# Kernel optimization log

Hardware: AMD Instinct MI355X
Metric: run time of the kernel (lower is better)

## Reference

```python
import jax, jax.numpy as jnp
import numpy as np


def _gelu(x):
    # torch.nn.functional.gelu default: exact erf form
    return jax.nn.gelu(x, approximate=False)


def setup_inputs() -> dict:
    key = jax.random.key(0)
    ks = jax.random.split(key, 6)
    B, L, H, MAXLEN = 8, 2048, 1024, 256
    former_input = jax.random.normal(ks[0], (B, L, H), dtype=jnp.float32)
    hidden_sates = jax.random.normal(ks[1], (B, L, H), dtype=jnp.float32)
    token_type_ids = jax.random.randint(ks[2], (B, L), 0, MAXLEN, dtype=jnp.int32)
    attention_mask = jnp.ones((B, L), dtype=jnp.float32)
    # learned params (init.normal_ std=0.02, biases zero)
    W_down = jax.random.normal(ks[3], (2 * H, H), dtype=jnp.float32) * 0.02
    b_down = jnp.zeros((H,), dtype=jnp.float32)
    W_row = jax.random.normal(ks[4], (H, H), dtype=jnp.float32) * 0.02
    b_row = jnp.zeros((H,), dtype=jnp.float32)
    return {
        "former_input": former_input,
        "hidden_sates": hidden_sates,
        "token_type_ids": token_type_ids,
        "attention_mask": attention_mask,
        "W_down": W_down,
        "b_down": b_down,
        "W_row": W_row,
        "b_row": b_row,
        "max_length": 256,
    }


def reference(former_input, hidden_sates, token_type_ids, attention_mask,
              W_down, b_down, W_row, b_row, max_length):
    # down_proj + gelu: [B, L, 2H] @ [2H, H] -> [B, L, H]
    x = jnp.concatenate([former_input, hidden_sates], axis=-1)
    sequence_output = _gelu(jnp.einsum("blf,fh->blh", x, W_down) + b_down)

    # one_hot_from @ sequence_output == segment-sum of tokens into table cells
    # cell_hidden[b, t] = sum_{l : token_type_ids[b,l]==t} sequence_output[b, l]
    seg = jax.vmap(lambda vals, ids: jax.ops.segment_sum(vals, ids, num_segments=max_length))
    cell_hidden = seg(sequence_output, token_type_ids)  # [B, max_length, H]

    # row_linear + gelu (dropout is identity in eval mode)
    cell_hidden = _gelu(jnp.einsum("bth,hk->btk", cell_hidden, W_row) + b_row)

    # one_hot_to @ cell_hidden == gather cell back to each token position
    seq_hidden = jnp.take_along_axis(
        cell_hidden, token_type_ids[:, :, None].astype(jnp.int32), axis=1
    )  # [B, L, H]
    return seq_hidden
```

## Files before the change

kernel.cpp:

```cpp
#include <hip/hip_runtime.h>

typedef unsigned short ushort_t;
typedef __bf16 bf16x8 __attribute__((ext_vector_type(8)));
typedef float f32x4 __attribute__((ext_vector_type(4)));

__device__ __forceinline__ unsigned short f2bf(float f) {
    unsigned u = __float_as_uint(f);
    u += 0x7fffu + ((u >> 16) & 1u);
    return (unsigned short)(u >> 16);
}
__device__ __forceinline__ float bf2f(unsigned short h) {
    return __uint_as_float(((unsigned)h) << 16);
}
__device__ __forceinline__ float gelu_f(float x) {
    return 0.5f * x * (1.0f + erff(x * 0.70710678118654752440f));
}

__global__ void prep_kernel(const float4* __restrict__ former,
                            const float4* __restrict__ hidden,
                            uint4* __restrict__ Xb4,
                            const float* __restrict__ Wd, ushort_t* __restrict__ WdT,
                            const float* __restrict__ Wr, ushort_t* __restrict__ WrT)
{
    const int blk = blockIdx.x;
    const int tid = threadIdx.x;
    if (blk < 16384) {
        const int row = blk;
        const float4* src = (tid < 128)
            ? (former + (size_t)row * 256 + (tid & 127) * 2)
            : (hidden + (size_t)row * 256 + (tid & 127) * 2);
        float4 a = src[0], b = src[1];
        uint4 o;
        o.x = f2bf(a.x) | ((unsigned)f2bf(a.y) << 16);
        o.y = f2bf(a.z) | ((unsigned)f2bf(a.w) << 16);
        o.z = f2bf(b.x) | ((unsigned)f2bf(b.y) << 16);
        o.w = f2bf(b.z) | ((unsigned)f2bf(b.w) << 16);
        Xb4[(size_t)row * 256 + tid] = o;
    } else {
        __shared__ float tile[32][33];
        const float* W; ushort_t* Wt; int R, C, b;
        if (blk < 16384 + 2048) { b = blk - 16384; W = Wd; Wt = WdT; R = 2048; C = 1024; }
        else                    { b = blk - 18432; W = Wr; Wt = WrT; R = 1024; C = 1024; }
        const int bx = (b & 31) * 32;
        const int by = (b >> 5) * 32;
        const int tx = tid & 31, ty = tid >> 5;
        #pragma unroll
        for (int j = 0; j < 32; j += 8)
            tile[ty + j][tx] = W[(size_t)(by + ty + j) * C + bx + tx];
        __syncthreads();
        #pragma unroll
        for (int j = 0; j < 32; j += 8)
            Wt[(size_t)(bx + ty + j) * R + by + tx] = f2bf(tile[tx][ty + j]);
    }
}

template <bool OUT_BF16>
__global__ void gemm_bias_gelu_kernel(const ushort_t* __restrict__ A,
                                      const ushort_t* __restrict__ Bt,
                                      const float* __restrict__ bias,
                                      void* __restrict__ C,
                                      int M, int N, int K)
{
    __shared__ __align__(16) ushort_t sA[128 * 64];
    __shared__ __align__(16) ushort_t sB[128 * 64];
    const int tid  = threadIdx.x;
    const int lane = tid & 63;
    const int wave = tid >> 6;
    const int wm = (wave & 1) * 64;
    const int wn = (wave >> 1) * 64;
    const long bm = (long)blockIdx.x * 128;
    const long bn = (long)blockIdx.y * 128;

    f32x4 acc[4][4] = {};

    const int srow = wave * 8 + (lane >> 3);
    const int scol = ((lane & 7) ^ (lane >> 3)) * 8;
    const int ldsbase = wave * 512;

    for (int k0 = 0; k0 < K; k0 += 64) {
        __syncthreads();
        #pragma unroll
        for (int it = 0; it < 4; ++it) {
            const ushort_t* gA = A + (size_t)(bm + it * 32 + srow) * K + k0 + scol;
            const ushort_t* gB = Bt + (size_t)(bn + it * 32 + srow) * K + k0 + scol;
            __builtin_amdgcn_global_load_lds(
                (__attribute__((address_space(1))) void*)gA,
                (__attribute__((address_space(3))) void*)&sA[ldsbase + it * 2048], 16, 0, 0);
            __builtin_amdgcn_global_load_lds(
                (__attribute__((address_space(1))) void*)gB,
                (__attribute__((address_space(3))) void*)&sB[ldsbase + it * 2048], 16, 0, 0);
        }
        __syncthreads();

        const int arow = wm + (lane & 15);
        const int brow = wn + (lane & 15);
        const int sw = lane & 7;
        const int cbase = lane >> 4;
        #pragma unroll
        for (int kk = 0; kk < 64; kk += 32) {
            const int koff = (((kk >> 3) + cbase) ^ sw) << 3;
            bf16x8 af[4], bfr[4];
            #pragma unroll
            for (int t = 0; t < 4; ++t) {
                af[t]  = *(const bf16x8*)&sA[(arow + t * 16) * 64 + koff];
                bfr[t] = *(const bf16x8*)&sB[(brow + t * 16) * 64 + koff];
            }
            #pragma unroll
            for (int i = 0; i < 4; ++i)
                #pragma unroll
                for (int j = 0; j < 4; ++j)
                    acc[i][j] = __builtin_amdgcn_mfma_f32_16x16x32_bf16(af[i], bfr[j], acc[i][j], 0, 0, 0);
        }
    }

    #pragma unroll
    for (int i = 0; i < 4; ++i) {
        const long row0 = bm + wm + i * 16 + (lane >> 4) * 4;
        #pragma unroll
        for (int j = 0; j < 4; ++j) {
            const long col = bn + wn + j * 16 + (lane & 15);
            const float bv = bias[col];
            #pragma unroll
            for (int r = 0; r < 4; ++r) {
                float v = gelu_f(acc[i][j][r] + bv);
                if (OUT_BF16)
                    ((ushort_t*)C)[(size_t)(row0 + r) * N + col] = f2bf(v);
                else
                    ((float*)C)[(size_t)(row0 + r) * N + col] = v;
            }
        }
    }
}

template <bool OUT_BF16>
__global__ __launch_bounds__(512, 2)
void gemm256_bias_gelu_kernel(const ushort_t* __restrict__ A,
                              const ushort_t* __restrict__ Bt,
                              const float* __restrict__ bias,
                              void* __restrict__ C,
                              int M, int N, int K)
{
    extern __shared__ float4 smem4[];
    ushort_t* sA = (ushort_t*)smem4;
    ushort_t* sB = sA + 32768;

    const int tid  = threadIdx.x;
    const int lane = tid & 63;
    const int w    = tid >> 6;
    const int wr   = w >> 2;
    const int wcq  = w & 3;
    const long bm = (long)blockIdx.x * 256;
    const long bn = (long)blockIdx.y * 256;
    const int NT = K >> 6;

    const int srow = w * 8 + (lane >> 3);
    const int scol = ((lane & 7) ^ (lane >> 3)) * 8;
    const int sdst = (lane & 7) * 8;

    const int l15 = lane & 15;
    const int lg  = lane >> 4;
    const int sw  = lane & 7;
    const int ck[2] = { ((0 + lg) ^ sw) * 8, ((4 + lg) ^ sw) * 8 };

    f32x4 acc[8][4] = {};

    auto stageA = [&](int t_, int mh_, int buf_) {
        #pragma unroll
        for (int j = 0; j < 2; ++j) {
            const ushort_t* g = A + (size_t)(bm + j * 128 + mh_ * 64 + srow) * K
                                  + t_ * 64 + scol;
            ushort_t* d = sA + buf_ * 16384 + mh_ * 8192 + (j * 64 + srow) * 64 + sdst;
            __builtin_amdgcn_global_load_lds(
                (__attribute__((address_space(1))) void*)g,
                (__attribute__((address_space(3))) void*)d, 16, 0, 0);
        }
    };
    auto stageB = [&](int t_, int nh_, int buf_) {
        #pragma unroll
        for (int j = 0; j < 2; ++j) {
            const ushort_t* g = Bt + (size_t)(bn + (j * 2 + wr) * 64 + nh_ * 32
                                              + (w & 3) * 8 + (lane >> 3)) * K
                                   + t_ * 64 + scol;
            ushort_t* d = sB + buf_ * 16384 + nh_ * 8192 + (j * 64 + srow) * 64 + sdst;
            __builtin_amdgcn_global_load_lds(
                (__attribute__((address_space(1))) void*)g,
                (__attribute__((address_space(3))) void*)d, 16, 0, 0);
        }
    };

    bf16x8 af[4][2];
    bf16x8 b0[2][2];
    bf16x8 b1[2][2];

    auto readA = [&](int mh_, int buf_) {
        #pragma unroll
        for (int tf = 0; tf < 4; ++tf)
            #pragma unroll
            for (int kk = 0; kk < 2; ++kk)
                af[tf][kk] = *(const bf16x8*)&sA[buf_ * 16384 + mh_ * 8192
                                + (wr * 64 + tf * 16 + l15) * 64 + ck[kk]];
    };
    auto readB = [&](bf16x8 (&dst)[2][2], int nh_, int buf_) {
        #pragma unroll
        for (int u = 0; u < 2; ++u)
            #pragma unroll
            for (int kk = 0; kk < 2; ++kk)
                dst[u][kk] = *(const bf16x8*)&sB[buf_ * 16384 + nh_ * 8192
                                + (wcq * 32 + u * 16 + l15) * 64 + ck[kk]];
    };
    auto mfma16 = [&](bf16x8 (&bf_)[2][2], int mh_, int nh_) {
        __builtin_amdgcn_s_setprio(1);
        #pragma unroll
        for (int tf = 0; tf < 4; ++tf)
            #pragma unroll
            for (int u = 0; u < 2; ++u) {
                acc[mh_ * 4 + tf][nh_ * 2 + u] =
                    __builtin_amdgcn_mfma_f32_16x16x32_bf16(
                        af[tf][0], bf_[u][0], acc[mh_ * 4 + tf][nh_ * 2 + u], 0, 0, 0);
                acc[mh_ * 4 + tf][nh_ * 2 + u] =
                    __builtin_amdgcn_mfma_f32_16x16x32_bf16(
                        af[tf][1], bf_[u][1], acc[mh_ * 4 + tf][nh_ * 2 + u], 0, 0, 0);
            }
        __builtin_amdgcn_s_setprio(0);
    };

    stageA(0, 0, 0); stageB(0, 0, 0);
    stageA(0, 1, 0); stageB(0, 1, 0);
    stageA(1, 0, 1); stageB(1, 0, 1);
    asm volatile("s_waitcnt vmcnt(4)" ::: "memory");

    for (int t2 = 0; t2 < NT; t2 += 2) {
        #pragma unroll
        for (int hIt = 0; hIt < 2; ++hIt) {
            const int t = t2 + hIt;
            const int cur = hIt;
            const bool lastt = (t == NT - 1);

            if (lastt) asm volatile("s_waitcnt vmcnt(0)" ::: "memory");
            else       asm volatile("s_waitcnt vmcnt(8)" ::: "memory");
            __builtin_amdgcn_s_barrier();
            if (t + 1 < NT) stageA(t + 1, 1, cur ^ 1);
            readA(0, cur);
            readB(b0, 0, cur);
            mfma16(b0, 0, 0);

            if (!lastt) asm volatile("s_waitcnt vmcnt(6)" ::: "memory");
            __builtin_amdgcn_s_barrier();
            if (t + 1 < NT) stageB(t + 1, 1, cur ^ 1);
            readB(b1, 1, cur);
            mfma16(b1, 0, 1);

            __builtin_amdgcn_s_barrier();
            if (t + 2 < NT) stageA(t + 2, 0, cur);
            readA(1, cur);
            mfma16(b0, 1, 0);

            __builtin_amdgcn_s_barrier();
            if (t + 2 < NT) stageB(t + 2, 0, cur);
            mfma16(b1, 1, 1);
        }
    }

    #pragma unroll
    for (int im = 0; im < 8; ++im) {
        const long row0 = bm + wr * 128 + (im >> 2) * 64 + (im & 3) * 16 + lg * 4;
        #pragma unroll
        for (int jn = 0; jn < 4; ++jn) {
            const long col = bn + wcq * 64 + jn * 16 + l15;
            const float bv = bias[col];
            #pragma unroll
            for (int r = 0; r < 4; ++r) {
                float v = gelu_f(acc[im][jn][r] + bv);
                if (OUT_BF16)
                    ((ushort_t*)C)[(size_t)(row0 + r) * N + col] = f2bf(v);
                else
                    ((float*)C)[(size_t)(row0 + r) * N + col] = v;
            }
        }
    }
}

__global__ void segsum_kernel(const ushort_t* __restrict__ seq,
                              const int* __restrict__ ids,
                              ushort_t* __restrict__ cell)
{
    const int b = blockIdx.x >> 8;
    const int t = blockIdx.x & 255;
    __shared__ int list[2048];
    __shared__ int count;
    if (threadIdx.x == 0) count = 0;
    __syncthreads();
    const int* idrow = ids + b * 2048;
    for (int l = threadIdx.x; l < 2048; l += 256) {
        if (idrow[l] == t) list[atomicAdd(&count, 1)] = l;
    }
    __syncthreads();
    const int n = count;
    float a0 = 0.f, a1 = 0.f, a2 = 0.f, a3 = 0.f;
    for (int i = 0; i < n; ++i) {
        const int l = list[i];
        const ushort4 v = *(const ushort4*)(seq + (size_t)(b * 2048 + l) * 1024 + threadIdx.x * 4);
        a0 += bf2f(v.x); a1 += bf2f(v.y); a2 += bf2f(v.z); a3 += bf2f(v.w);
    }
    ushort4* out = (ushort4*)(cell + (size_t)(b * 256 + t) * 1024);
    out[threadIdx.x] = make_ushort4(f2bf(a0), f2bf(a1), f2bf(a2), f2bf(a3));
}

__global__ void gather_kernel(const float4* __restrict__ cellout,
                              const int* __restrict__ ids,
                              float4* __restrict__ out)
{
    const int tok = blockIdx.x;
    const int b = tok >> 11;
    const int t = ids[tok];
    out[(size_t)tok * 256 + threadIdx.x] = cellout[(size_t)(b * 256 + t) * 256 + threadIdx.x];
}

extern "C" void kernel_launch(void* const* d_in, const int* in_sizes, int n_in,
                              void* d_out, int out_size, void* d_ws, size_t ws_size,
                              hipStream_t stream) {
    const float* former = (const float*)d_in[0];
    const float* hidden = (const float*)d_in[1];
    const int*   ids    = (const int*)d_in[2];
    const float* W_down = (const float*)d_in[4];
    const float* b_down = (const float*)d_in[5];
    const float* W_row  = (const float*)d_in[6];
    const float* b_row  = (const float*)d_in[7];
    float* out = (float*)d_out;

    char* ws = (char*)d_ws;
    ushort_t* Xb    = (ushort_t*)ws;  ws += (size_t)16384 * 2048 * 2;
    ushort_t* WdT   = (ushort_t*)ws;  ws += (size_t)1024 * 2048 * 2;
    ushort_t* WrT   = (ushort_t*)ws;  ws += (size_t)1024 * 1024 * 2;
    ushort_t* seq   = (ushort_t*)ws;  ws += (size_t)16384 * 1024 * 2;
    ushort_t* cellb = (ushort_t*)ws;  ws += (size_t)2048 * 1024 * 2;
    float*    cello = (float*)ws;

    static bool s_attr_set = false;
    if (!s_attr_set) {
        hipFuncSetAttribute(reinterpret_cast<const void*>(&gemm256_bias_gelu_kernel<true>),
                            hipFuncAttributeMaxDynamicSharedMemorySize, 131072);
        s_attr_set = true;
    }

    prep_kernel<<<19456, 256, 0, stream>>>((const float4*)former, (const float4*)hidden,
                                           (uint4*)Xb, W_down, WdT, W_row, WrT);

    gemm256_bias_gelu_kernel<true><<<dim3(64, 4), 512, 131072, stream>>>(
        Xb, WdT, b_down, seq, 16384, 1024, 2048);

    segsum_kernel<<<2048, 256, 0, stream>>>(seq, ids, cellb);

    gemm_bias_gelu_kernel<false><<<dim3(16, 8), 256, 0, stream>>>(cellb, WrT, b_row, cello,
                                                                  2048, 1024, 1024);
    gather_kernel<<<16384, 256, 0, stream>>>((const float4*)cello, ids, (float4*)out);
}
```

Measured before the change: 321.4 us.

## Restructure GEMM main loop into ping-pong phases with separate A fragment registers

Splits the A-fragment registers into two sets so both halves of the A tile can be held at once. The main loop is rearranged into phases of LDS reads plus prefetch issue, then a barrier, then an MFMA cluster wrapped in sched_barrier and more barriers. The aim is to separate memory and compute phases cleanly across waves and to hide global-to-LDS latency. It adds registers and many extra barriers, and the changed vmcnt accounting risks stalls or correctness issues in the buffer hand-off.

```diff
diff --git a/kernel.cpp b/kernel.cpp
--- a/kernel.cpp
+++ b/kernel.cpp
@@ -188,16 +188,17 @@
         }
     };
 
-    bf16x8 af[4][2];
+    bf16x8 af0[4][2];
+    bf16x8 af1[4][2];
     bf16x8 b0[2][2];
     bf16x8 b1[2][2];
 
-    auto readA = [&](int mh_, int buf_) {
+    auto readA = [&](bf16x8 (&dst)[4][2], int mh_, int buf_) {
         #pragma unroll
         for (int tf = 0; tf < 4; ++tf)
             #pragma unroll
             for (int kk = 0; kk < 2; ++kk)
-                af[tf][kk] = *(const bf16x8*)&sA[buf_ * 16384 + mh_ * 8192
+                dst[tf][kk] = *(const bf16x8*)&sA[buf_ * 16384 + mh_ * 8192
                                 + (wr * 64 + tf * 16 + l15) * 64 + ck[kk]];
     };
     auto readB = [&](bf16x8 (&dst)[2][2], int nh_, int buf_) {
@@ -208,7 +209,7 @@
                 dst[u][kk] = *(const bf16x8*)&sB[buf_ * 16384 + nh_ * 8192
                                 + (wcq * 32 + u * 16 + l15) * 64 + ck[kk]];
     };
-    auto mfma16 = [&](bf16x8 (&bf_)[2][2], int mh_, int nh_) {
+    auto mfma16 = [&](bf16x8 (&a_)[4][2], bf16x8 (&bf_)[2][2], int mh_, int nh_) {
         __builtin_amdgcn_s_setprio(1);
         #pragma unroll
         for (int tf = 0; tf < 4; ++tf)
@@ -216,10 +217,10 @@
             for (int u = 0; u < 2; ++u) {
                 acc[mh_ * 4 + tf][nh_ * 2 + u] =
                     __builtin_amdgcn_mfma_f32_16x16x32_bf16(
-                        af[tf][0], bf_[u][0], acc[mh_ * 4 + tf][nh_ * 2 + u], 0, 0, 0);
+                        a_[tf][0], bf_[u][0], acc[mh_ * 4 + tf][nh_ * 2 + u], 0, 0, 0);
                 acc[mh_ * 4 + tf][nh_ * 2 + u] =
                     __builtin_amdgcn_mfma_f32_16x16x32_bf16(
-                        af[tf][1], bf_[u][1], acc[mh_ * 4 + tf][nh_ * 2 + u], 0, 0, 0);
+                        a_[tf][1], bf_[u][1], acc[mh_ * 4 + tf][nh_ * 2 + u], 0, 0, 0);
             }
         __builtin_amdgcn_s_setprio(0);
     };
@@ -227,37 +228,53 @@
     stageA(0, 0, 0); stageB(0, 0, 0);
     stageA(0, 1, 0); stageB(0, 1, 0);
     stageA(1, 0, 1); stageB(1, 0, 1);
-    asm volatile("s_waitcnt vmcnt(4)" ::: "memory");
+    asm volatile("s_waitcnt vmcnt(8)" ::: "memory");
+    __builtin_amdgcn_s_barrier();
 
     for (int t2 = 0; t2 < NT; t2 += 2) {
         #pragma unroll
         for (int hIt = 0; hIt < 2; ++hIt) {
             const int t = t2 + hIt;
             const int cur = hIt;
-            const bool lastt = (t == NT - 1);
-
-            if (lastt) asm volatile("s_waitcnt vmcnt(0)" ::: "memory");
-            else       asm volatile("s_waitcnt vmcnt(8)" ::: "memory");
-            __builtin_amdgcn_s_barrier();
-            if (t + 1 < NT) stageA(t + 1, 1, cur ^ 1);
-            readA(0, cur);
+
+            readA(af0, 0, cur);
             readB(b0, 0, cur);
-            mfma16(b0, 0, 0);
-
-            if (!lastt) asm volatile("s_waitcnt vmcnt(6)" ::: "memory");
-            __builtin_amdgcn_s_barrier();
+            if (t + 1 < NT) {
+                stageA(t + 1, 1, cur ^ 1);
+                asm volatile("s_waitcnt vmcnt(6)" ::: "memory");
+            }
+            asm volatile("s_waitcnt lgkmcnt(8)" ::: "memory");
+            __builtin_amdgcn_s_barrier();
+            asm volatile("s_waitcnt lgkmcnt(0)" ::: "memory");
+            __builtin_amdgcn_sched_barrier(0);
+            mfma16(af0, b0, 0, 0);
+            __builtin_amdgcn_s_barrier();
+
+            readB(b1, 1, cur);
             if (t + 1 < NT) stageB(t + 1, 1, cur ^ 1);
-            readB(b1, 1, cur);
-            mfma16(b1, 0, 1);
-
-            __builtin_amdgcn_s_barrier();
+            __builtin_amdgcn_s_barrier();
+            asm volatile("s_waitcnt lgkmcnt(0)" ::: "memory");
+            __builtin_amdgcn_sched_barrier(0);
+            mfma16(af0, b1, 0, 1);
+            __builtin_amdgcn_s_barrier();
+
+            readA(af1, 1, cur);
             if (t + 2 < NT) stageA(t + 2, 0, cur);
-            readA(1, cur);
-            mfma16(b0, 1, 0);
-
-            __builtin_amdgcn_s_barrier();
-            if (t + 2 < NT) stageB(t + 2, 0, cur);
-            mfma16(b1, 1, 1);
+            __builtin_amdgcn_s_barrier();
+            asm volatile("s_waitcnt lgkmcnt(0)" ::: "memory");
+            __builtin_amdgcn_sched_barrier(0);
+            mfma16(af1, b0, 1, 0);
+            __builtin_amdgcn_s_barrier();
+
+            if (t + 2 < NT) {
+                stageB(t + 2, 0, cur);
+                asm volatile("s_waitcnt vmcnt(8)" ::: "memory");
+            } else if (t + 1 < NT) {
+                asm volatile("s_waitcnt vmcnt(0)" ::: "memory");
+            }
+            __builtin_amdgcn_s_barrier();
+            mfma16(af1, b1, 1, 1);
+            __builtin_amdgcn_s_barrier();
         }
     }
 
```

Result: no change. 323.0 us (+0.5%).
